# Optimization experiments

Hardware: AMD Instinct MI355X
Metric: run time of the kernel (lower is better)

Reference implementation:

```python
import jax, jax.numpy as jnp
import numpy as np

D_MODEL = 768
N_HEAD = 12
N_BR = 4
DH = D_MODEL // N_HEAD          # 64
H_TOT = N_BR * N_HEAD           # 48
K_TOP = 4
B, T = 2, 1024


def setup_inputs() -> dict:
    key = jax.random.key(0)
    ks = jax.random.split(key, 16)
    s = 0.02
    return {
        "A": jax.random.normal(ks[0], (B, T, D_MODEL), jnp.float32),
        "X": jax.random.normal(ks[1], (B, T, D_MODEL), jnp.float32),
        "WK_w": jax.random.normal(ks[2], (D_MODEL, D_MODEL), jnp.float32) * s,
        "WK_b": jax.random.normal(ks[3], (D_MODEL,), jnp.float32) * s,
        "WQ_w": jax.random.normal(ks[4], (D_MODEL * N_BR, D_MODEL), jnp.float32) * s,
        "wedge_A": jax.random.normal(ks[5], (DH, DH), jnp.float32) * s,
        "wedge_bias": jax.random.normal(ks[6], (H_TOT, DH), jnp.float32) * s,
        "sink": jax.random.normal(ks[7], (H_TOT,), jnp.float32) * s,
        "v_nulls": jax.random.normal(ks[8], (N_BR, D_MODEL), jnp.float32) * s,
        "V1_w": jax.random.normal(ks[9], (4 * DH, DH), jnp.float32) * s,
        "V1_b": jax.random.normal(ks[10], (4 * DH,), jnp.float32) * s,
        "V2_w": jax.random.normal(ks[11], (DH, 4 * DH), jnp.float32) * s,
        "V2_b": jax.random.normal(ks[12], (DH,), jnp.float32) * s,
        "WO_w": jax.random.normal(ks[13], (N_BR, D_MODEL, D_MODEL), jnp.float32) * s,
        "WO_b": jax.random.normal(ks[14], (N_BR, D_MODEL), jnp.float32) * s,
    }


def _wedge(x, wedge_A, wedge_bias):
    # S = (A - A^T) + diag_embed(id_bias); x: [B,H,T,Dh]
    skew = wedge_A - wedge_A.T                       # [Dh,Dh]
    S = skew[None, :, :] + jax.vmap(jnp.diag)(wedge_bias)  # [H,Dh,Dh]
    return x + jnp.einsum('bhtd,hde->bhte', x, S)


def _rope(x):
    # x: [B,H,T,Dh]; halves are interleaved-split then concatenated
    t_len = x.shape[2]
    inv_freq = 1.0 / (10000.0 ** (jnp.arange(0, DH, 2, dtype=jnp.float32) / DH))
    freqs = jnp.arange(t_len, dtype=jnp.float32)[:, None] * inv_freq[None, :]  # [T,Dh/2]
    cos = jnp.cos(freqs)[None, None]
    sin = jnp.sin(freqs)[None, None]
    x1 = x[..., 0::2]
    x2 = x[..., 1::2]
    return jnp.concatenate((-x2 * sin + x1 * cos, x1 * sin + x2 * cos), axis=-1)


def reference(A, X, WK_w, WK_b, WQ_w, wedge_A, wedge_bias, sink, v_nulls,
              V1_w, V1_b, V2_w, V2_b, WO_w, WO_b):
    b, t, c = A.shape
    scale = DH ** -0.5

    q = (A @ WQ_w.T).reshape(b, t, H_TOT, DH).transpose(0, 2, 1, 3)     # [B,Htot,T,Dh]
    k_base = X @ WK_w.T + WK_b
    k = k_base.reshape(b, t, N_HEAD, DH).transpose(0, 2, 1, 3)          # [B,Nsh,T,Dh]
    k = jnp.tile(k, (1, N_BR, 1, 1))                                    # [B,Htot,T,Dh]

    q = _rope(_wedge(q, wedge_A, wedge_bias))
    k = _rope(_wedge(k, wedge_A, wedge_bias))

    scores = jnp.einsum('bhtd,bhsd->bhts', q, k) * scale                # [B,Htot,T,T]
    causal = jnp.triu(jnp.ones((t, t), dtype=bool), k=1)
    scores = jnp.where(causal[None, None], -jnp.inf, scores)

    sinks = jnp.broadcast_to(sink.reshape(1, H_TOT, 1, 1), (b, H_TOT, t, 1))
    probs_full = jax.nn.softmax(jnp.concatenate([scores, sinks], axis=-1), axis=-1)
    probs_tokens = probs_full[..., :t]
    probs_sink = probs_full[..., t:]                                    # [B,Htot,T,1]

    k_top = min(K_TOP, t)
    vals, idxs = jax.lax.top_k(probs_tokens, k_top)                     # [B,Htot,T,K]
    weights = vals / (jnp.sum(vals, axis=-1, keepdims=True) + 1e-9)

    # gather top-k keys: [B,Htot,T,K,Dh]
    k_selected = jnp.take_along_axis(k[:, :, None, :, :], idxs[..., None], axis=3)
    marker = jnp.einsum('bhtk,bhtkd->bhtd', weights, k_selected)        # [B,Htot,T,Dh]

    h = jax.nn.gelu(marker @ V1_w.T + V1_b, approximate=False)
    out_tokens = h @ V2_w.T + V2_b                                      # [B,Htot,T,Dh]

    v_null = v_nulls.reshape(H_TOT, DH)[None, :, None, :]
    context = out_tokens + probs_sink * v_null                          # [B,Htot,T,Dh]

    context = context.reshape(b, N_BR, N_HEAD, t, DH)
    context = context.transpose(0, 1, 3, 2, 4).reshape(b, N_BR, t, c)   # [B,Nbr,T,C]

    y = jnp.einsum('bntc,ncd->bntd', context, WO_w) + WO_b[None, :, None, :]
    return y.mean(axis=1)
```

## Files before the change

kernel.cpp:

```cpp
#include <hip/hip_runtime.h>
#include <math.h>

constexpr int Bq  = 2;
constexpr int Tq  = 1024;
constexpr int HTq = 48;
constexpr float SCALE = 0.125f;
constexpr float EOFF = 8.0f;

typedef __attribute__((ext_vector_type(8))) short short8;
typedef __attribute__((ext_vector_type(4))) float f32x4;

__device__ inline unsigned short f2bf(float x) {
    unsigned u = __float_as_uint(x);
    return (unsigned short)((u + 0x7FFF + ((u >> 16) & 1)) >> 16);
}

__device__ inline unsigned umax_(unsigned a, unsigned b) { return a > b ? a : b; }
__device__ inline unsigned umin_(unsigned a, unsigned b) { return a > b ? b : a; }

__device__ inline void gload_lds16(const unsigned short* g, unsigned short* l) {
    __builtin_amdgcn_global_load_lds(
        (const __attribute__((address_space(1))) void*)g,
        (__attribute__((address_space(3))) void*)l,
        16, 0, 0);
}

__device__ inline void split3(float x, unsigned short& p0, unsigned short& p1, unsigned short& p2) {
    p0 = f2bf(x);
    float f0 = __uint_as_float((unsigned)p0 << 16);
    float r0 = x - f0;
    p1 = f2bf(r0);
    float f1 = __uint_as_float((unsigned)p1 << 16);
    float r1 = r0 - f1;
    p2 = f2bf(r1);
}

__device__ inline float gelu_f(float x) {
    float z = 0.70710678118654752f * x;
    float az = fabsf(z);
    float t = __frcp_rn(1.0f + 0.3275911f * az);
    float poly = t * (0.254829592f + t * (-0.284496736f + t * (1.421413741f
               + t * (-1.453152027f + t * 1.061405429f))));
    float er = 1.0f - poly * __expf(-az * az);
    er = (z < 0.0f) ? -er : er;
    return 0.5f * x * (1.0f + er);
}

__global__ void trig_kbias_kernel(float* __restrict__ trig,
                                  const float* __restrict__ WKb,
                                  const float* __restrict__ wA,
                                  float* __restrict__ bcat) {
    int i = blockIdx.x * 256 + threadIdx.x;
    int t = i >> 5, f = i & 31;
    float invf = powf(10000.0f, -(float)f * (1.0f / 32.0f));
    float ang = (float)t * invf;
    trig[i] = cosf(ang);
    trig[32768 + i] = sinf(ang);
    if (i < 768) {
        int hb = i >> 6, el = i & 63;
        float acc = 0.0f;
        for (int d = 0; d < 64; d++) {
            float sk = wA[d * 64 + el] - wA[el * 64 + d];
            acc += WKb[hb * 64 + d] * sk;
        }
        bcat[i] = WKb[i] + acc;
    } else if (i < 1536) {
        bcat[i] = WKb[i - 768];
    }
}

__global__ __launch_bounds__(256) void fold_split_kernel(
    const float* __restrict__ WQw, const float* __restrict__ WKw,
    const float* __restrict__ wA, const float* __restrict__ wbias,
    unsigned short* __restrict__ Wsp)
{
    const size_t WPL = (size_t)4608 * 768;
    __shared__ float sw[64][132];
    __shared__ float sk[64][65];
    int hb_ = blockIdx.x;
    int mode = (hb_ < 48) ? 0 : 1;
    int h = mode ? hb_ - 48 : hb_;
    const float* Wsrc = mode ? WKw : WQw;
    int cb = blockIdx.y;
    int tid = threadIdx.x;
    const float* Wh = Wsrc + (size_t)h * 64 * 768 + cb * 128;
    for (int l = tid; l < 64 * 32; l += 256) {
        int d = l >> 5, c4 = l & 31;
        *(float4*)&sw[d][c4 * 4] = *(const float4*)(Wh + (size_t)d * 768 + c4 * 4);
    }
    for (int l = tid; l < 4096; l += 256) {
        int d = l >> 6, e = l & 63;
        sk[d][e] = wA[l] - wA[e * 64 + d];
    }
    __syncthreads();
    int tx = tid & 15, ty = tid >> 4;
    float acc4[4][8] = {};
    for (int d = 0; d < 64; d++) {
        float s0 = sk[d][ty * 4 + 0], s1 = sk[d][ty * 4 + 1];
        float s2 = sk[d][ty * 4 + 2], s3 = sk[d][ty * 4 + 3];
        float w_[8];
        *(float4*)&w_[0] = *(const float4*)&sw[d][tx * 8];
        *(float4*)&w_[4] = *(const float4*)&sw[d][tx * 8 + 4];
        #pragma unroll
        for (int j = 0; j < 8; j++) {
            acc4[0][j] += s0 * w_[j];
            acc4[1][j] += s1 * w_[j];
            acc4[2][j] += s2 * w_[j];
            acc4[3][j] += s3 * w_[j];
        }
    }
    #pragma unroll
    for (int i = 0; i < 4; i++) {
        int e = ty * 4 + i;
        float scale = (mode == 0) ? (1.0f + wbias[h * 64 + e]) : 1.0f;
        size_t row = (mode == 0) ? (size_t)(h * 64 + e) : (size_t)(3072 + h * 64 + e);
        #pragma unroll
        for (int j = 0; j < 8; j++) {
            int cl = tx * 8 + j;
            float wv = sw[e][cl] * scale + acc4[i][j];
            unsigned short p0, p1, p2;
            split3(wv, p0, p1, p2);
            size_t idx = row * 768 + cb * 128 + cl;
            Wsp[idx] = p0; Wsp[WPL + idx] = p1; Wsp[2 * WPL + idx] = p2;
        }
        if (mode == 1) {
            size_t row2 = (size_t)(3840 + h * 64 + e);
            #pragma unroll
            for (int j = 0; j < 8; j++) {
                int cl = tx * 8 + j;
                unsigned short p0, p1, p2;
                split3(sw[e][cl], p0, p1, p2);
                size_t idx = row2 * 768 + cb * 128 + cl;
                Wsp[idx] = p0; Wsp[WPL + idx] = p1; Wsp[2 * WPL + idx] = p2;
            }
        }
    }
}

__global__ void split_act_kernel(const float* __restrict__ A, const float* __restrict__ X,
                                 unsigned short* __restrict__ Asp, unsigned short* __restrict__ Xsp)
{
    const size_t APL = (size_t)2048 * 768;
    int i = blockIdx.x * 256 + threadIdx.x;
    if (i >= 393216) return;
    float4 va = ((const float4*)A)[i];
    float4 vx = ((const float4*)X)[i];
    ushort4 a0, a1, a2, x0, x1, x2;
    split3(va.x, a0.x, a1.x, a2.x); split3(va.y, a0.y, a1.y, a2.y);
    split3(va.z, a0.z, a1.z, a2.z); split3(va.w, a0.w, a1.w, a2.w);
    split3(vx.x, x0.x, x1.x, x2.x); split3(vx.y, x0.y, x1.y, x2.y);
    split3(vx.z, x0.z, x1.z, x2.z); split3(vx.w, x0.w, x1.w, x2.w);
    ((ushort4*)(Asp))[i] = a0;
    ((ushort4*)(Asp + APL))[i] = a1;
    ((ushort4*)(Asp + 2 * APL))[i] = a2;
    ((ushort4*)(Xsp))[i] = x0;
    ((ushort4*)(Xsp + APL))[i] = x1;
    ((ushort4*)(Xsp + 2 * APL))[i] = x2;
}

__global__ __launch_bounds__(512) void proj_mfma_kernel(
    const unsigned short* __restrict__ Asp, const unsigned short* __restrict__ Xsp,
    const unsigned short* __restrict__ Wsp, const float* __restrict__ bcat,
    const float* __restrict__ trig, float* __restrict__ Qr, float* __restrict__ O2)
{
    const size_t APL = (size_t)2048 * 768;
    const size_t WPL = (size_t)4608 * 768;
    __shared__ unsigned short sA[3 * 128 * 32];
    __shared__ unsigned short sB[3 * 128 * 32];
    int bid = blockIdx.x;
    int swz = (bid & 7) * 72 + (bid >> 3);
    int nb = swz >> 4;
    int mb = swz & 15;
    bool isQ = (nb < 24);
    const unsigned short* Ab = isQ ? Asp : Xsp;
    int m0 = mb * 128, n0 = nb * 128;
    int tid = threadIdx.x;
    int w = tid >> 6, lane = tid & 63;
    int wm = w & 1, wn = w >> 1;
    int rf = lane & 15, kg = lane >> 4;
    int mbase = m0 + wm * 64;

    int srcslot = (lane & 3) ^ ((lane >> 3) & 3);
    const unsigned short* gsrcA[3];
    const unsigned short* gsrcB[3];
    unsigned short* ldstA[3];
    unsigned short* ldstB[3];
    #pragma unroll
    for (int i = 0; i < 3; i++) {
        int reg = w + i * 8;
        int p = reg >> 3, rg = reg & 7;
        int row = rg * 16 + (lane >> 2);
        gsrcA[i] = Ab  + (size_t)p * APL + (size_t)(m0 + row) * 768 + srcslot * 8;
        gsrcB[i] = Wsp + (size_t)p * WPL + (size_t)(n0 + row) * 768 + srcslot * 8;
        ldstA[i] = &sA[p * 4096 + rg * 512];
        ldstB[i] = &sB[p * 4096 + rg * 512];
    }

    f32x4 acc[4][2] = {};
    for (int k0 = 0; k0 < 768; k0 += 32) {
        __syncthreads();
        #pragma unroll
        for (int i = 0; i < 3; i++) {
            gload_lds16(gsrcA[i] + k0, ldstA[i]);
            gload_lds16(gsrcB[i] + k0, ldstB[i]);
        }
        __syncthreads();

        short8 a0[4], a1[4], a2[4], b0[2], b1[2], b2[2];
        #pragma unroll
        for (int mi = 0; mi < 4; mi++) {
            int row = wm * 64 + mi * 16 + rf;
            a0[mi] = *(const short8*)&sA[0 * 4096 + row * 32 + ((kg ^ ((row >> 1) & 3)) * 8)];
        }
        #pragma unroll
        for (int nj = 0; nj < 2; nj++) {
            int row = wn * 32 + nj * 16 + rf;
            b0[nj] = *(const short8*)&sB[0 * 4096 + row * 32 + ((kg ^ ((row >> 1) & 3)) * 8)];
        }
        #pragma unroll
        for (int mi = 0; mi < 4; mi++)
            #pragma unroll
            for (int nj = 0; nj < 2; nj++)
                acc[mi][nj] = __builtin_amdgcn_mfma_f32_16x16x32_bf16(a0[mi], b0[nj], acc[mi][nj], 0, 0, 0);
        #pragma unroll
        for (int nj = 0; nj < 2; nj++) {
            int row = wn * 32 + nj * 16 + rf;
            b1[nj] = *(const short8*)&sB[1 * 4096 + row * 32 + ((kg ^ ((row >> 1) & 3)) * 8)];
        }
        #pragma unroll
        for (int mi = 0; mi < 4; mi++)
            #pragma unroll
            for (int nj = 0; nj < 2; nj++)
                acc[mi][nj] = __builtin_amdgcn_mfma_f32_16x16x32_bf16(a0[mi], b1[nj], acc[mi][nj], 0, 0, 0);
        #pragma unroll
        for (int nj = 0; nj < 2; nj++) {
            int row = wn * 32 + nj * 16 + rf;
            b2[nj] = *(const short8*)&sB[2 * 4096 + row * 32 + ((kg ^ ((row >> 1) & 3)) * 8)];
        }
        #pragma unroll
        for (int mi = 0; mi < 4; mi++)
            #pragma unroll
            for (int nj = 0; nj < 2; nj++)
                acc[mi][nj] = __builtin_amdgcn_mfma_f32_16x16x32_bf16(a0[mi], b2[nj], acc[mi][nj], 0, 0, 0);
        #pragma unroll
        for (int mi = 0; mi < 4; mi++) {
            int row = wm * 64 + mi * 16 + rf;
            a1[mi] = *(const short8*)&sA[1 * 4096 + row * 32 + ((kg ^ ((row >> 1) & 3)) * 8)];
        }
        #pragma unroll
        for (int mi = 0; mi < 4; mi++)
            #pragma unroll
            for (int nj = 0; nj < 2; nj++)
                acc[mi][nj] = __builtin_amdgcn_mfma_f32_16x16x32_bf16(a1[mi], b0[nj], acc[mi][nj], 0, 0, 0);
        #pragma unroll
        for (int mi = 0; mi < 4; mi++)
            #pragma unroll
            for (int nj = 0; nj < 2; nj++)
                acc[mi][nj] = __builtin_amdgcn_mfma_f32_16x16x32_bf16(a1[mi], b1[nj], acc[mi][nj], 0, 0, 0);
        #pragma unroll
        for (int mi = 0; mi < 4; mi++) {
            int row = wm * 64 + mi * 16 + rf;
            a2[mi] = *(const short8*)&sA[2 * 4096 + row * 32 + ((kg ^ ((row >> 1) & 3)) * 8)];
        }
        #pragma unroll
        for (int mi = 0; mi < 4; mi++)
            #pragma unroll
            for (int nj = 0; nj < 2; nj++)
                acc[mi][nj] = __builtin_amdgcn_mfma_f32_16x16x32_bf16(a2[mi], b0[nj], acc[mi][nj], 0, 0, 0);
    }

    if (isQ) {
        #pragma unroll
        for (int mi = 0; mi < 4; mi++) {
            #pragma unroll
            for (int r = 0; r < 4; r++) {
                int m = mbase + mi * 16 + kg * 4 + r;
                int b_ = m >> 10, t = m & 1023;
                #pragma unroll
                for (int nj = 0; nj < 2; nj++) {
                    int col_local = wn * 32 + nj * 16 + rf;
                    int h = nb * 2 + (col_local >> 6);
                    int d = col_local & 63;
                    int i = d >> 1;
                    float v = acc[mi][nj][r];
                    float pv = __shfl_xor(v, 1);
                    float c = trig[t * 32 + i];
                    float s = trig[32768 + t * 32 + i];
                    float outv = (rf & 1) ? (pv * s + v * c) : (v * c - pv * s);
                    int col = (rf & 1) ? (32 + i) : i;
                    size_t base = ((size_t)(b_ * 48 + h) * 1024 + t) * 64;
                    Qr[base + col] = outv;
                }
            }
        }
    } else {
        #pragma unroll
        for (int nj = 0; nj < 2; nj++) {
            int col = (n0 - 3072) + wn * 32 + nj * 16 + rf;
            float bv = bcat[col];
            #pragma unroll
            for (int mi = 0; mi < 4; mi++)
                #pragma unroll
                for (int r = 0; r < 4; r++) {
                    int m = mbase + mi * 16 + kg * 4 + r;
                    O2[(size_t)m * 1536 + col] = acc[mi][nj][r] + bv;
                }
        }
    }
}

__global__ void k_finish_kernel(const float* __restrict__ O2, const float* __restrict__ trig,
                                const float* __restrict__ wbias,
                                float* __restrict__ Kr, unsigned short* __restrict__ Kb16)
{
    int idx = blockIdx.x * 256 + threadIdx.x;
    int pr = idx & 31;
    int tmp = idx >> 5;
    int hb = tmp % 12;
    int bt = tmp / 12;
    int t = bt & 1023, b = bt >> 10;
    const float* yx = O2 + (size_t)bt * 1536 + hb * 64 + pr * 2;
    float y0 = yx[0], y1 = yx[1];
    float x0 = yx[768], x1 = yx[769];
    float cv = trig[t * 32 + pr], sv = trig[32768 + t * 32 + pr];
    #pragma unroll
    for (int r = 0; r < 4; r++) {
        int h = hb + 12 * r;
        float b0 = wbias[h * 64 + 2 * pr], b1 = wbias[h * 64 + 2 * pr + 1];
        float wz0 = y0 + x0 * b0;
        float wz1 = y1 + x1 * b1;
        float lo = wz0 * cv - wz1 * sv;
        float hi = wz0 * sv + wz1 * cv;
        size_t base = ((size_t)(b * 48 + h) * 1024 + t) * 64;
        Kr[base + pr] = lo;
        Kr[base + 32 + pr] = hi;
        Kb16[base + pr] = f2bf(lo);
        Kb16[base + 32 + pr] = f2bf(hi);
    }
}

__global__ __launch_bounds__(256, 4) void attn_mfma_topk_kernel(
    const float* __restrict__ Qr, const float* __restrict__ Kr,
    const unsigned short* __restrict__ Kb, const float* __restrict__ sink,
    unsigned short* __restrict__ markerb, float* __restrict__ psink)
{
    const int bh = blockIdx.x;
    const int y  = blockIdx.y;
    const int w = threadIdx.x >> 6, lane = threadIdx.x & 63;
    const int rf = lane & 15, kg = lane >> 4;
    const int h = bh % HTq;
    const size_t rowbase = (size_t)bh * Tq;
    const unsigned short* Kbb = Kb + rowbase * 64;
    const float sk = sink[h];

    #pragma unroll 1
    for (int g = 0; g < 2; g++) {
        const int qb = g ? y : 15 - y;
        const int q0 = qb * 64 + w * 16;

        short8 a0, a1;
        {
            const float* qp = Qr + (rowbase + q0 + rf) * 64 + kg * 8;
            float4 u0 = *(const float4*)qp;
            float4 u1 = *(const float4*)(qp + 4);
            float4 u2 = *(const float4*)(qp + 32);
            float4 u3 = *(const float4*)(qp + 36);
            a0[0]=(short)f2bf(u0.x); a0[1]=(short)f2bf(u0.y); a0[2]=(short)f2bf(u0.z); a0[3]=(short)f2bf(u0.w);
            a0[4]=(short)f2bf(u1.x); a0[5]=(short)f2bf(u1.y); a0[6]=(short)f2bf(u1.z); a0[7]=(short)f2bf(u1.w);
            a1[0]=(short)f2bf(u2.x); a1[1]=(short)f2bf(u2.y); a1[2]=(short)f2bf(u2.z); a1[3]=(short)f2bf(u2.w);
            a1[4]=(short)f2bf(u3.x); a1[5]=(short)f2bf(u3.y); a1[6]=(short)f2bf(u3.z); a1[7]=(short)f2bf(u3.w);
        }

        float Z_[4];
        unsigned t_[4][4];
        #pragma unroll
        for (int r = 0; r < 4; r++) {
            Z_[r] = 0.0f;
            t_[r][0] = 0u; t_[r][1] = 0u; t_[r][2] = 0u; t_[r][3] = 0u;
        }

        short8 cA0[4], cA1[4], cB0[4], cB1[4];
        {
            const unsigned short* p = Kbb + (size_t)rf * 64 + kg * 8;
            #pragma unroll
            for (int kc = 0; kc < 4; kc++) {
                cA0[kc] = *(const short8*)(p + kc * 1024);
                cA1[kc] = *(const short8*)(p + kc * 1024 + 32);
            }
        }

        auto body = [&](short8 (&cb0)[4], short8 (&cb1)[4],
                        short8 (&nb0)[4], short8 (&nb1)[4], int tile) {
            f32x4 accs[4];
            __builtin_amdgcn_s_setprio(1);
            #pragma unroll
            for (int kc = 0; kc < 4; kc++) {
                f32x4 acc = {0.f, 0.f, 0.f, 0.f};
                acc = __builtin_amdgcn_mfma_f32_16x16x32_bf16(a0, cb0[kc], acc, 0, 0, 0);
                acc = __builtin_amdgcn_mfma_f32_16x16x32_bf16(a1, cb1[kc], acc, 0, 0, 0);
                accs[kc] = acc;
            }
            __builtin_amdgcn_s_setprio(0);
            const unsigned short* np = Kbb + (size_t)((tile + 1) * 64 + rf) * 64 + kg * 8;
            #pragma unroll
            for (int kc = 0; kc < 4; kc++) {
                nb0[kc] = *(const short8*)(np + kc * 1024);
                nb1[kc] = *(const short8*)(np + kc * 1024 + 32);
            }
            const int s0 = tile << 6;
            #pragma unroll
            for (int r = 0; r < 4; r++) {
                float s8[4];
                #pragma unroll
                for (int kc = 0; kc < 4; kc++) s8[kc] = fmaf(accs[kc][r], SCALE, -EOFF);
                #pragma unroll
                for (int kc = 0; kc < 4; kc++) {
                    unsigned u = __float_as_uint(s8[kc]);
                    unsigned key = u ^ ((unsigned)(((int)u) >> 31) | 0x80000000u);
                    unsigned c = (key & 0xFFFFFC00u) | (unsigned)(s0 + kc * 16 + rf);
                    unsigned n;
                    n = umax_(t_[r][0], c);  c = umin_(t_[r][0], c);  t_[r][0] = n;
                    n = umax_(t_[r][1], c);  c = umin_(t_[r][1], c);  t_[r][1] = n;
                    n = umax_(t_[r][2], c);  c = umin_(t_[r][2], c);  t_[r][2] = n;
                    t_[r][3] = umax_(t_[r][3], c);
                }
                float e0 = __expf(s8[0]), e1 = __expf(s8[1]);
                float e2 = __expf(s8[2]), e3 = __expf(s8[3]);
                Z_[r] += (e0 + e1) + (e2 + e3);
            }
        };

        int tile = 0;
        for (; tile + 1 < qb; tile += 2) {
            body(cA0, cA1, cB0, cB1, tile);
            body(cB0, cB1, cA0, cA1, tile + 1);
        }
        if (tile < qb) {
            body(cA0, cA1, cB0, cB1, tile);
            #pragma unroll
            for (int kc = 0; kc < 4; kc++) { cA0[kc] = cB0[kc]; cA1[kc] = cB1[kc]; }
        }

        {
            f32x4 accs[4];
            __builtin_amdgcn_s_setprio(1);
            #pragma unroll
            for (int kc = 0; kc < 4; kc++) {
                f32x4 acc = {0.f, 0.f, 0.f, 0.f};
                acc = __builtin_amdgcn_mfma_f32_16x16x32_bf16(a0, cA0[kc], acc, 0, 0, 0);
                acc = __builtin_amdgcn_mfma_f32_16x16x32_bf16(a1, cA1[kc], acc, 0, 0, 0);
                accs[kc] = acc;
            }
            __builtin_amdgcn_s_setprio(0);
            const int s0 = qb << 6;
            #pragma unroll
            for (int r = 0; r < 4; r++) {
                const int trow = q0 + kg * 4 + r;
                float ev[4];
                #pragma unroll
                for (int kc = 0; kc < 4; kc++) {
                    int k = s0 + kc * 16 + rf;
                    bool ok = (k <= trow);
                    float s8 = fmaf(accs[kc][r], SCALE, -EOFF);
                    unsigned u = __float_as_uint(s8);
                    unsigned key = u ^ ((unsigned)(((int)u) >> 31) | 0x80000000u);
                    unsigned c = (key & 0xFFFFFC00u) | (unsigned)k;
                    c = ok ? c : 0u;
                    unsigned n;
                    n = umax_(t_[r][0], c);  c = umin_(t_[r][0], c);  t_[r][0] = n;
                    n = umax_(t_[r][1], c);  c = umin_(t_[r][1], c);  t_[r][1] = n;
                    n = umax_(t_[r][2], c);  c = umin_(t_[r][2], c);  t_[r][2] = n;
                    t_[r][3] = umax_(t_[r][3], c);
                    ev[kc] = ok ? __expf(s8) : 0.0f;
                }
                Z_[r] += (ev[0] + ev[1]) + (ev[2] + ev[3]);
            }
        }

        const float esk = __expf(sk - EOFF);
        #pragma unroll 1
        for (int r = 0; r < 4; r++) {
            const int q = q0 + kg * 4 + r;
            float Z = Z_[r];
            #pragma unroll
            for (int off = 1; off < 16; off <<= 1) Z += __shfl_xor(Z, off);
            float Zf = Z + esk;

            unsigned e0, e1, e2, e3, e4, e5, e6, e7;
            {
                unsigned A0 = t_[r][0], A1 = t_[r][1], A2 = t_[r][2], A3 = t_[r][3];
                unsigned B0 = (unsigned)__shfl_xor((int)A0, 1);
                unsigned B1 = (unsigned)__shfl_xor((int)A1, 1);
                unsigned B2 = (unsigned)__shfl_xor((int)A2, 1);
                unsigned B3 = (unsigned)__shfl_xor((int)A3, 1);
                unsigned y0 = umax_(A0, B3), y4 = umin_(A0, B3);
                unsigned y1 = umax_(A1, B2), y5 = umin_(A1, B2);
                unsigned y2 = umax_(A2, B1), y6 = umin_(A2, B1);
                unsigned y3 = umax_(A3, B0), y7 = umin_(A3, B0);
                unsigned z0 = umax_(y0, y2), z2 = umin_(y0, y2);
                unsigned z1 = umax_(y1, y3), z3 = umin_(y1, y3);
                unsigned z4 = umax_(y4, y6), z6 = umin_(y4, y6);
                unsigned z5 = umax_(y5, y7), z7 = umin_(y5, y7);
                e0 = umax_(z0, z1); e1 = umin_(z0, z1);
                e2 = umax_(z2, z3); e3 = umin_(z2, z3);
                e4 = umax_(z4, z5); e5 = umin_(z4, z5);
                e6 = umax_(z6, z7); e7 = umin_(z6, z7);
            }
            auto merge8 = [&](int off) {
                unsigned f0 = (unsigned)__shfl_xor((int)e0, off);
                unsigned f1 = (unsigned)__shfl_xor((int)e1, off);
                unsigned f2 = (unsigned)__shfl_xor((int)e2, off);
                unsigned f3 = (unsigned)__shfl_xor((int)e3, off);
                unsigned f4 = (unsigned)__shfl_xor((int)e4, off);
                unsigned f5 = (unsigned)__shfl_xor((int)e5, off);
                unsigned f6 = (unsigned)__shfl_xor((int)e6, off);
                unsigned f7 = (unsigned)__shfl_xor((int)e7, off);
                unsigned m0 = umax_(e0, f7), m1 = umax_(e1, f6);
                unsigned m2 = umax_(e2, f5), m3 = umax_(e3, f4);
                unsigned m4 = umax_(e4, f3), m5 = umax_(e5, f2);
                unsigned m6 = umax_(e6, f1), m7 = umax_(e7, f0);
                unsigned p0 = umax_(m0, m4), p4 = umin_(m0, m4);
                unsigned p1 = umax_(m1, m5), p5 = umin_(m1, m5);
                unsigned p2 = umax_(m2, m6), p6 = umin_(m2, m6);
                unsigned p3 = umax_(m3, m7), p7 = umin_(m3, m7);
                unsigned q0_ = umax_(p0, p2), q2_ = umin_(p0, p2);
                unsigned q1_ = umax_(p1, p3), q3_ = umin_(p1, p3);
                unsigned q4_ = umax_(p4, p6), q6_ = umin_(p4, p6);
                unsigned q5_ = umax_(p5, p7), q7_ = umin_(p5, p7);
                e0 = umax_(q0_, q1_); e1 = umin_(q0_, q1_);
                e2 = umax_(q2_, q3_); e3 = umin_(q2_, q3_);
                e4 = umax_(q4_, q5_); e5 = umin_(q4_, q5_);
                e6 = umax_(q6_, q7_); e7 = umin_(q6_, q7_);
            };
            merge8(2); merge8(4); merge8(8);
            unsigned ck[8] = {e0, e1, e2, e3, e4, e5, e6, e7};

            const float4 qv = *(const float4*)(Qr + (rowbase + q) * 64 + rf * 4);
            float sc[8]; int ci[8];
            #pragma unroll
            for (int c = 0; c < 8; c++) {
                bool valid = (ck[c] != 0u);
                int idx = (int)(ck[c] & 1023u);
                int lidx = valid ? idx : 0;
                const float4 kv = *(const float4*)(Kr + (rowbase + lidx) * 64 + rf * 4);
                float p = qv.x * kv.x + qv.y * kv.y + qv.z * kv.z + qv.w * kv.w;
                #pragma unroll
                for (int off = 1; off < 16; off <<= 1) p += __shfl_xor(p, off);
                sc[c] = valid ? p * SCALE : -1e30f;
                ci[c] = valid ? idx : -1;
            }
            float bv[4]; int bi[4];
            #pragma unroll
            for (int rd = 0; rd < 4; rd++) {
                float v = sc[0]; int id = ci[0];
                #pragma unroll
                for (int c = 1; c < 8; c++) {
                    bool take = (sc[c] > v) || ((sc[c] == v) && ((unsigned)ci[c] < (unsigned)id));
                    v = take ? sc[c] : v; id = take ? ci[c] : id;
                }
                bv[rd] = v; bi[rd] = id;
                #pragma unroll
                for (int c = 0; c < 8; c++) {
                    bool kill = (ci[c] == id) && (sc[c] == v);
                    sc[c] = kill ? -3e30f : sc[c];
                }
            }
            float e0f = __expf(bv[0] - EOFF), e1f = __expf(bv[1] - EOFF);
            float e2f = __expf(bv[2] - EOFF), e3f = __expf(bv[3] - EOFF);
            float wsum = e0f + e1f + e2f + e3f + Zf * 1e-9f;
            float w0 = e0f / wsum, w1 = e1f / wsum, w2 = e2f / wsum, w3 = e3f / wsum;
            int i0 = bi[0] < 0 ? 0 : bi[0];
            int i1 = bi[1] < 0 ? 0 : bi[1];
            int i2 = bi[2] < 0 ? 0 : bi[2];
            int i3 = bi[3] < 0 ? 0 : bi[3];
            const float4 k0 = *(const float4*)(Kr + (rowbase + i0) * 64 + rf * 4);
            const float4 k1 = *(const float4*)(Kr + (rowbase + i1) * 64 + rf * 4);
            const float4 k2 = *(const float4*)(Kr + (rowbase + i2) * 64 + rf * 4);
            const float4 k3 = *(const float4*)(Kr + (rowbase + i3) * 64 + rf * 4);
            float mx = w0 * k0.x + w1 * k1.x + w2 * k2.x + w3 * k3.x;
            float my = w0 * k0.y + w1 * k1.y + w2 * k2.y + w3 * k3.y;
            float mz = w0 * k0.z + w1 * k1.z + w2 * k2.z + w3 * k3.z;
            float mw = w0 * k0.w + w1 * k1.w + w2 * k2.w + w3 * k3.w;
            ushort4 mo;
            mo.x = f2bf(mx); mo.y = f2bf(my); mo.z = f2bf(mz); mo.w = f2bf(mw);
            *(ushort4*)(markerb + (rowbase + q) * 64 + rf * 4) = mo;
            if (rf == 0) psink[rowbase + q] = esk / Zf;
        }
    }
}

__global__ void cvt_bf16_kernel(const float* __restrict__ V1w, const float* __restrict__ V2w,
                                unsigned short* __restrict__ outb)
{
    int i = blockIdx.x * 256 + threadIdx.x;
    if (i >= 8192) return;
    float4 v = (i < 4096) ? ((const float4*)V1w)[i] : ((const float4*)V2w)[i - 4096];
    ushort4 o;
    o.x = f2bf(v.x); o.y = f2bf(v.y); o.z = f2bf(v.z); o.w = f2bf(v.w);
    ((ushort4*)outb)[i] = o;
}

__global__ __launch_bounds__(256) void wo_transpose_kernel(
    const float* __restrict__ WOw, unsigned short* __restrict__ WOt)
{
    __shared__ float tl[64][65];
    int tid = threadIdx.x;
    int n = blockIdx.z;
    int c0 = blockIdx.x * 64, d0 = blockIdx.y * 64;
    const float* src = WOw + (size_t)n * 768 * 768;
    for (int l = tid; l < 64 * 16; l += 256) {
        int r = l >> 4, q = l & 15;
        float4 v = *(const float4*)(src + (size_t)(c0 + r) * 768 + d0 + q * 4);
        tl[r][q * 4 + 0] = v.x; tl[r][q * 4 + 1] = v.y;
        tl[r][q * 4 + 2] = v.z; tl[r][q * 4 + 3] = v.w;
    }
    __syncthreads();
    for (int l = tid; l < 64 * 16; l += 256) {
        int d = l >> 4, q = l & 15;
        ushort4 o;
        o.x = f2bf(tl[q * 4 + 0][d]); o.y = f2bf(tl[q * 4 + 1][d]);
        o.z = f2bf(tl[q * 4 + 2][d]); o.w = f2bf(tl[q * 4 + 3][d]);
        *(ushort4*)(WOt + (size_t)n * 768 * 768 + (size_t)(d0 + d) * 768 + c0 + q * 4) = o;
    }
}

__global__ __launch_bounds__(256) void mlp_mfma_kernel(
    const unsigned short* __restrict__ markerb, const float* __restrict__ psink,
    const unsigned short* __restrict__ V1b16, const float* __restrict__ V1bias,
    const unsigned short* __restrict__ V2b16, const float* __restrict__ V2bias,
    const float* __restrict__ vnulls, unsigned short* __restrict__ ctxb)
{
    __shared__ float h_lds[4][16][65];
    int tid = threadIdx.x;
    int w = tid >> 6, lane = tid & 63;
    int rf = lane & 15, kg = lane >> 4;
    size_t r0 = (size_t)blockIdx.x * 64 + 16 * w;

    short8 a1[2];
    #pragma unroll
    for (int kk = 0; kk < 2; kk++)
        a1[kk] = *(const short8*)(markerb + (r0 + rf) * 64 + kk * 32 + kg * 8);

    f32x4 acc2[4] = {};
    for (int ch = 0; ch < 4; ch++) {
        f32x4 acc1[4] = {};
        #pragma unroll
        for (int nj = 0; nj < 4; nj++)
            #pragma unroll
            for (int kk = 0; kk < 2; kk++) {
                short8 b1 = *(const short8*)(V1b16 + (size_t)(ch * 64 + nj * 16 + rf) * 64 + kk * 32 + kg * 8);
                acc1[nj] = __builtin_amdgcn_mfma_f32_16x16x32_bf16(a1[kk], b1, acc1[nj], 0, 0, 0);
            }
        __syncthreads();
        #pragma unroll
        for (int nj = 0; nj < 4; nj++) {
            float bb = V1bias[ch * 64 + nj * 16 + rf];
            #pragma unroll
            for (int r = 0; r < 4; r++) {
                float x = acc1[nj][r] + bb;
                h_lds[w][kg * 4 + r][nj * 16 + rf] = gelu_f(x);
            }
        }
        __syncthreads();
        #pragma unroll
        for (int kk = 0; kk < 2; kk++) {
            const float* hp = &h_lds[w][rf][kk * 32 + kg * 8];
            float4 p0 = *(const float4*)hp;
            float4 p1 = *(const float4*)(hp + 4);
            short8 a2;
            a2[0] = (short)f2bf(p0.x); a2[1] = (short)f2bf(p0.y);
            a2[2] = (short)f2bf(p0.z); a2[3] = (short)f2bf(p0.w);
            a2[4] = (short)f2bf(p1.x); a2[5] = (short)f2bf(p1.y);
            a2[6] = (short)f2bf(p1.z); a2[7] = (short)f2bf(p1.w);
            #pragma unroll
            for (int njo = 0; njo < 4; njo++) {
                short8 b2 = *(const short8*)(V2b16 + (size_t)(njo * 16 + rf) * 256 + ch * 64 + kk * 32 + kg * 8);
                acc2[njo] = __builtin_amdgcn_mfma_f32_16x16x32_bf16(a2, b2, acc2[njo], 0, 0, 0);
            }
        }
    }
    #pragma unroll
    for (int r = 0; r < 4; r++) {
        size_t R = r0 + kg * 4 + r;
        int bh = (int)(R >> 10), t = (int)(R & 1023);
        int b = bh / 48, h = bh % 48;
        int n = h / 12, head = h % 12;
        float ps = psink[R];
        size_t base = ((size_t)((b * 4 + n) * 1024 + t)) * 768 + head * 64;
        #pragma unroll
        for (int njo = 0; njo < 4; njo++) {
            int d = njo * 16 + rf;
            float v = acc2[njo][r] + V2bias[d] + ps * vnulls[h * 64 + d];
            ctxb[base + d] = f2bf(v);
        }
    }
}

__global__ __launch_bounds__(256) void gemm_wo_mfma(
    const unsigned short* __restrict__ ctxb, const unsigned short* __restrict__ WOtb,
    const float* __restrict__ WOb, float* __restrict__ Out)
{
    __shared__ unsigned short sA[64 * 64];
    __shared__ unsigned short sB[64 * 64];
    int tid = threadIdx.x;
    int w = tid >> 6, lane = tid & 63;
    int wm = w >> 1, wn = w & 1;
    int rf = lane & 15, kg = lane >> 4;
    int m0 = blockIdx.x * 64, n0 = blockIdx.y * 64;
    int b = m0 >> 10, t0 = m0 & 1023;
    int c0 = tid * 2, c1 = tid * 2 + 1;
    int ra = c0 >> 3, ca = c0 & 7, rb = c1 >> 3, cb = c1 & 7;
    f32x4 acc[2][2] = {};
    for (int n = 0; n < 4; n++) {
        const unsigned short* Ab = ctxb + ((size_t)((b * 4 + n) * 1024 + t0)) * 768;
        const unsigned short* Bb = WOtb + (size_t)n * 768 * 768 + (size_t)n0 * 768;
        for (int k0 = 0; k0 < 768; k0 += 64) {
            __syncthreads();
            *(short8*)&sA[ra * 64 + ((ca ^ (ra & 7)) * 8)] = *(const short8*)(Ab + (size_t)ra * 768 + k0 + ca * 8);
            *(short8*)&sA[rb * 64 + ((cb ^ (rb & 7)) * 8)] = *(const short8*)(Ab + (size_t)rb * 768 + k0 + cb * 8);
            *(short8*)&sB[ra * 64 + ((ca ^ (ra & 7)) * 8)] = *(const short8*)(Bb + (size_t)ra * 768 + k0 + ca * 8);
            *(short8*)&sB[rb * 64 + ((cb ^ (rb & 7)) * 8)] = *(const short8*)(Bb + (size_t)rb * 768 + k0 + cb * 8);
            __syncthreads();
            #pragma unroll
            for (int kk = 0; kk < 2; kk++) {
                int kc = kk * 4 + kg;
                int rA0 = wm * 32 + rf, rA1 = wm * 32 + 16 + rf;
                int rB0 = wn * 32 + rf, rB1 = wn * 32 + 16 + rf;
                short8 a0v = *(const short8*)&sA[rA0 * 64 + ((kc ^ (rA0 & 7)) * 8)];
                short8 a1v = *(const short8*)&sA[rA1 * 64 + ((kc ^ (rA1 & 7)) * 8)];
                short8 b0v = *(const short8*)&sB[rB0 * 64 + ((kc ^ (rB0 & 7)) * 8)];
                short8 b1v = *(const short8*)&sB[rB1 * 64 + ((kc ^ (rB1 & 7)) * 8)];
                acc[0][0] = __builtin_amdgcn_mfma_f32_16x16x32_bf16(a0v, b0v, acc[0][0], 0, 0, 0);
                acc[0][1] = __builtin_amdgcn_mfma_f32_16x16x32_bf16(a0v, b1v, acc[0][1], 0, 0, 0);
                acc[1][0] = __builtin_amdgcn_mfma_f32_16x16x32_bf16(a1v, b0v, acc[1][0], 0, 0, 0);
                acc[1][1] = __builtin_amdgcn_mfma_f32_16x16x32_bf16(a1v, b1v, acc[1][1], 0, 0, 0);
            }
        }
    }
    #pragma unroll
    for (int nj = 0; nj < 2; nj++) {
        int col = n0 + wn * 32 + nj * 16 + rf;
        float bm = WOb[col] + WOb[768 + col] + WOb[1536 + col] + WOb[2304 + col];
        #pragma unroll
        for (int mi = 0; mi < 2; mi++)
            #pragma unroll
            for (int r = 0; r < 4; r++) {
                int row = m0 + wm * 32 + mi * 16 + kg * 4 + r;
                Out[(size_t)row * 768 + col] = 0.25f * (acc[mi][nj][r] + bm);
            }
    }
}

extern "C" void kernel_launch(void* const* d_in, const int* in_sizes, int n_in,
                              void* d_out, int out_size, void* d_ws, size_t ws_size,
                              hipStream_t stream) {
    const float* A      = (const float*)d_in[0];
    const float* X      = (const float*)d_in[1];
    const float* WKw    = (const float*)d_in[2];
    const float* WKb    = (const float*)d_in[3];
    const float* WQw    = (const float*)d_in[4];
    const float* wA     = (const float*)d_in[5];
    const float* wB     = (const float*)d_in[6];
    const float* sink   = (const float*)d_in[7];
    const float* vnulls = (const float*)d_in[8];
    const float* V1w    = (const float*)d_in[9];
    const float* V1b    = (const float*)d_in[10];
    const float* V2w    = (const float*)d_in[11];
    const float* V2b    = (const float*)d_in[12];
    const float* WOw    = (const float*)d_in[13];
    const float* WOb    = (const float*)d_in[14];
    float* out = (float*)d_out;
    (void)in_sizes; (void)n_in; (void)out_size; (void)ws_size;

    float* ws = (float*)d_ws;
    size_t off = 0;
    float* Qr   = ws + off;  off += 6291456;
    float* Kr   = ws + off;  off += 6291456;
    float* trig = ws + off;  off += 65536;
    float* bcat = ws + off;  off += 2048;
    float* O2   = ws + off;  off += 3145728;
    float* Wsp_f = ws + off; off += 5308416;
    unsigned short* Wsp = (unsigned short*)Wsp_f;
    unsigned short* Asp = (unsigned short*)(ws + off); off += 2359296;
    unsigned short* Xsp = (unsigned short*)(ws + off); off += 2359296;
    unsigned short* markerb = (unsigned short*)O2;
    unsigned short* Kb16 = Wsp;
    float* psink = Wsp_f + 3145728;
    unsigned short* V1b16 = Xsp;
    unsigned short* V2b16 = V1b16 + 16384;
    unsigned short* WOtb  = Asp;
    unsigned short* ctxb  = (unsigned short*)Qr;

    trig_kbias_kernel<<<128, 256, 0, stream>>>(trig, WKb, wA, bcat);
    fold_split_kernel<<<dim3(60, 6), 256, 0, stream>>>(WQw, WKw, wA, wB, Wsp);
    split_act_kernel<<<1536, 256, 0, stream>>>(A, X, Asp, Xsp);
    proj_mfma_kernel<<<576, 512, 0, stream>>>(Asp, Xsp, Wsp, bcat, trig, Qr, O2);
    k_finish_kernel<<<3072, 256, 0, stream>>>(O2, trig, wB, Kr, Kb16);
    attn_mfma_topk_kernel<<<dim3(96, 8), 256, 0, stream>>>(Qr, Kr, Kb16, sink, markerb, psink);
    cvt_bf16_kernel<<<32, 256, 0, stream>>>(V1w, V2w, V1b16);
    wo_transpose_kernel<<<dim3(12, 12, 4), 256, 0, stream>>>(WOw, WOtb);
    mlp_mfma_kernel<<<1536, 256, 0, stream>>>(markerb, psink, V1b16, V1b, V2b16, V2b, vnulls, ctxb);
    gemm_wo_mfma<<<dim3(32, 12), 256, 0, stream>>>(ctxb, WOtb, WOb, out);
}
```

Before: 323.6 us.

## Fold bf16 weight conversion into setup kernel, drop MLP barriers, widen WO k-tile

Moves the V1/V2 bf16 conversion into the trig/bias setup kernel, which removes one launch, and gives the converted weights their own workspace slot. Removes the two block-wide barriers in the MLP kernel, since each wave only touches its own h_lds slice, and adds s_setprio around the MFMA bursts. Doubles the WO GEMM k-tile to 128 with a 16-way XOR swizzle, halving the number of barrier-separated load phases at the cost of more LDS per block.

```diff
diff --git a/kernel.cpp b/kernel.cpp
--- a/kernel.cpp
+++ b/kernel.cpp
@@ -49,7 +49,10 @@
 __global__ void trig_kbias_kernel(float* __restrict__ trig,
                                   const float* __restrict__ WKb,
                                   const float* __restrict__ wA,
-                                  float* __restrict__ bcat) {
+                                  float* __restrict__ bcat,
+                                  const float* __restrict__ V1w,
+                                  const float* __restrict__ V2w,
+                                  unsigned short* __restrict__ vb16) {
     int i = blockIdx.x * 256 + threadIdx.x;
     int t = i >> 5, f = i & 31;
     float invf = powf(10000.0f, -(float)f * (1.0f / 32.0f));
@@ -66,6 +69,12 @@
         bcat[i] = WKb[i] + acc;
     } else if (i < 1536) {
         bcat[i] = WKb[i - 768];
+    }
+    if (i < 8192) {
+        float4 v = (i < 4096) ? ((const float4*)V1w)[i] : ((const float4*)V2w)[i - 4096];
+        ushort4 o;
+        o.x = f2bf(v.x); o.y = f2bf(v.y); o.z = f2bf(v.z); o.w = f2bf(v.w);
+        ((ushort4*)vb16)[i] = o;
     }
 }
 
@@ -589,17 +598,6 @@
     }
 }
 
-__global__ void cvt_bf16_kernel(const float* __restrict__ V1w, const float* __restrict__ V2w,
-                                unsigned short* __restrict__ outb)
-{
-    int i = blockIdx.x * 256 + threadIdx.x;
-    if (i >= 8192) return;
-    float4 v = (i < 4096) ? ((const float4*)V1w)[i] : ((const float4*)V2w)[i - 4096];
-    ushort4 o;
-    o.x = f2bf(v.x); o.y = f2bf(v.y); o.z = f2bf(v.z); o.w = f2bf(v.w);
-    ((ushort4*)outb)[i] = o;
-}
-
 __global__ __launch_bounds__(256) void wo_transpose_kernel(
     const float* __restrict__ WOw, unsigned short* __restrict__ WOt)
 {
@@ -644,6 +642,7 @@
     f32x4 acc2[4] = {};
     for (int ch = 0; ch < 4; ch++) {
         f32x4 acc1[4] = {};
+        __builtin_amdgcn_s_setprio(1);
         #pragma unroll
         for (int nj = 0; nj < 4; nj++)
             #pragma unroll
@@ -651,7 +650,7 @@
                 short8 b1 = *(const short8*)(V1b16 + (size_t)(ch * 64 + nj * 16 + rf) * 64 + kk * 32 + kg * 8);
                 acc1[nj] = __builtin_amdgcn_mfma_f32_16x16x32_bf16(a1[kk], b1, acc1[nj], 0, 0, 0);
             }
-        __syncthreads();
+        __builtin_amdgcn_s_setprio(0);
         #pragma unroll
         for (int nj = 0; nj < 4; nj++) {
             float bb = V1bias[ch * 64 + nj * 16 + rf];
@@ -661,7 +660,6 @@
                 h_lds[w][kg * 4 + r][nj * 16 + rf] = gelu_f(x);
             }
         }
-        __syncthreads();
         #pragma unroll
         for (int kk = 0; kk < 2; kk++) {
             const float* hp = &h_lds[w][rf][kk * 32 + kg * 8];
@@ -672,11 +670,13 @@
             a2[2] = (short)f2bf(p0.z); a2[3] = (short)f2bf(p0.w);
             a2[4] = (short)f2bf(p1.x); a2[5] = (short)f2bf(p1.y);
             a2[6] = (short)f2bf(p1.z); a2[7] = (short)f2bf(p1.w);
+            __builtin_amdgcn_s_setprio(1);
             #pragma unroll
             for (int njo = 0; njo < 4; njo++) {
                 short8 b2 = *(const short8*)(V2b16 + (size_t)(njo * 16 + rf) * 256 + ch * 64 + kk * 32 + kg * 8);
                 acc2[njo] = __builtin_amdgcn_mfma_f32_16x16x32_bf16(a2, b2, acc2[njo], 0, 0, 0);
             }
+            __builtin_amdgcn_s_setprio(0);
         }
     }
     #pragma unroll
@@ -700,41 +700,45 @@
     const unsigned short* __restrict__ ctxb, const unsigned short* __restrict__ WOtb,
     const float* __restrict__ WOb, float* __restrict__ Out)
 {
-    __shared__ unsigned short sA[64 * 64];
-    __shared__ unsigned short sB[64 * 64];
+    __shared__ unsigned short sA[64 * 128];
+    __shared__ unsigned short sB[64 * 128];
     int tid = threadIdx.x;
     int w = tid >> 6, lane = tid & 63;
     int wm = w >> 1, wn = w & 1;
     int rf = lane & 15, kg = lane >> 4;
     int m0 = blockIdx.x * 64, n0 = blockIdx.y * 64;
     int b = m0 >> 10, t0 = m0 & 1023;
-    int c0 = tid * 2, c1 = tid * 2 + 1;
-    int ra = c0 >> 3, ca = c0 & 7, rb = c1 >> 3, cb = c1 & 7;
     f32x4 acc[2][2] = {};
     for (int n = 0; n < 4; n++) {
         const unsigned short* Ab = ctxb + ((size_t)((b * 4 + n) * 1024 + t0)) * 768;
         const unsigned short* Bb = WOtb + (size_t)n * 768 * 768 + (size_t)n0 * 768;
-        for (int k0 = 0; k0 < 768; k0 += 64) {
+        for (int k0 = 0; k0 < 768; k0 += 128) {
             __syncthreads();
-            *(short8*)&sA[ra * 64 + ((ca ^ (ra & 7)) * 8)] = *(const short8*)(Ab + (size_t)ra * 768 + k0 + ca * 8);
-            *(short8*)&sA[rb * 64 + ((cb ^ (rb & 7)) * 8)] = *(const short8*)(Ab + (size_t)rb * 768 + k0 + cb * 8);
-            *(short8*)&sB[ra * 64 + ((ca ^ (ra & 7)) * 8)] = *(const short8*)(Bb + (size_t)ra * 768 + k0 + ca * 8);
-            *(short8*)&sB[rb * 64 + ((cb ^ (rb & 7)) * 8)] = *(const short8*)(Bb + (size_t)rb * 768 + k0 + cb * 8);
+            #pragma unroll
+            for (int j = 0; j < 4; j++) {
+                int e = tid + j * 256;
+                int r = e >> 4, s = e & 15;
+                int ss = s ^ (r & 15);
+                *(short8*)&sA[r * 128 + ss * 8] = *(const short8*)(Ab + (size_t)r * 768 + k0 + s * 8);
+                *(short8*)&sB[r * 128 + ss * 8] = *(const short8*)(Bb + (size_t)r * 768 + k0 + s * 8);
+            }
             __syncthreads();
-            #pragma unroll
-            for (int kk = 0; kk < 2; kk++) {
-                int kc = kk * 4 + kg;
+            __builtin_amdgcn_s_setprio(1);
+            #pragma unroll
+            for (int kk = 0; kk < 4; kk++) {
+                int slot = kk * 4 + kg;
                 int rA0 = wm * 32 + rf, rA1 = wm * 32 + 16 + rf;
                 int rB0 = wn * 32 + rf, rB1 = wn * 32 + 16 + rf;
-                short8 a0v = *(const short8*)&sA[rA0 * 64 + ((kc ^ (rA0 & 7)) * 8)];
-                short8 a1v = *(const short8*)&sA[rA1 * 64 + ((kc ^ (rA1 & 7)) * 8)];
-                short8 b0v = *(const short8*)&sB[rB0 * 64 + ((kc ^ (rB0 & 7)) * 8)];
-                short8 b1v = *(const short8*)&sB[rB1 * 64 + ((kc ^ (rB1 & 7)) * 8)];
+                short8 a0v = *(const short8*)&sA[rA0 * 128 + ((slot ^ (rA0 & 15)) * 8)];
+                short8 a1v = *(const short8*)&sA[rA1 * 128 + ((slot ^ (rA1 & 15)) * 8)];
+                short8 b0v = *(const short8*)&sB[rB0 * 128 + ((slot ^ (rB0 & 15)) * 8)];
+                short8 b1v = *(const short8*)&sB[rB1 * 128 + ((slot ^ (rB1 & 15)) * 8)];
                 acc[0][0] = __builtin_amdgcn_mfma_f32_16x16x32_bf16(a0v, b0v, acc[0][0], 0, 0, 0);
                 acc[0][1] = __builtin_amdgcn_mfma_f32_16x16x32_bf16(a0v, b1v, acc[0][1], 0, 0, 0);
                 acc[1][0] = __builtin_amdgcn_mfma_f32_16x16x32_bf16(a1v, b0v, acc[1][0], 0, 0, 0);
                 acc[1][1] = __builtin_amdgcn_mfma_f32_16x16x32_bf16(a1v, b1v, acc[1][1], 0, 0, 0);
             }
+            __builtin_amdgcn_s_setprio(0);
         }
     }
     #pragma unroll
@@ -783,21 +787,20 @@
     unsigned short* Wsp = (unsigned short*)Wsp_f;
     unsigned short* Asp = (unsigned short*)(ws + off); off += 2359296;
     unsigned short* Xsp = (unsigned short*)(ws + off); off += 2359296;
+    unsigned short* V1b16 = (unsigned short*)(ws + off); off += 16384;
+    unsigned short* V2b16 = V1b16 + 16384;
     unsigned short* markerb = (unsigned short*)O2;
     unsigned short* Kb16 = Wsp;
     float* psink = Wsp_f + 3145728;
-    unsigned short* V1b16 = Xsp;
-    unsigned short* V2b16 = V1b16 + 16384;
     unsigned short* WOtb  = Asp;
     unsigned short* ctxb  = (unsigned short*)Qr;
 
-    trig_kbias_kernel<<<128, 256, 0, stream>>>(trig, WKb, wA, bcat);
+    trig_kbias_kernel<<<128, 256, 0, stream>>>(trig, WKb, wA, bcat, V1w, V2w, V1b16);
     fold_split_kernel<<<dim3(60, 6), 256, 0, stream>>>(WQw, WKw, wA, wB, Wsp);
     split_act_kernel<<<1536, 256, 0, stream>>>(A, X, Asp, Xsp);
     proj_mfma_kernel<<<576, 512, 0, stream>>>(Asp, Xsp, Wsp, bcat, trig, Qr, O2);
     k_finish_kernel<<<3072, 256, 0, stream>>>(O2, trig, wB, Kr, Kb16);
     attn_mfma_topk_kernel<<<dim3(96, 8), 256, 0, stream>>>(Qr, Kr, Kb16, sink, markerb, psink);
-    cvt_bf16_kernel<<<32, 256, 0, stream>>>(V1w, V2w, V1b16);
     wo_transpose_kernel<<<dim3(12, 12, 4), 256, 0, stream>>>(WOw, WOtb);
     mlp_mfma_kernel<<<1536, 256, 0, stream>>>(markerb, psink, V1b16, V1b, V2b16, V2b, vnulls, ctxb);
     gemm_wo_mfma<<<dim3(32, 12), 256, 0, stream>>>(ctxb, WOtb, WOb, out);
```

After: 315.8 us. 2.4% less time.
